# Performance work log

Measured on AMD Instinct MI355X. Metric: run time of the kernel, lower is better.

Reference implementation:

```python
import jax, jax.numpy as jnp
import numpy as np

B, L, H, HKV, D, E = 2, 2048, 8, 1, 256, 2048
SCALING = D ** -0.5


def rotate_half(x):
    x1, x2 = jnp.split(x, 2, axis=-1)
    return jnp.concatenate([-x2, x1], axis=-1)


def setup_inputs() -> dict:
    key = jax.random.key(0)
    ks = jax.random.split(key, 5)
    hidden_states = jax.random.normal(ks[0], (B, L, E), jnp.float32)
    attention_mask = jnp.zeros((B, 1, 1, L, L), jnp.float32)  # additive mask (all visible)
    # standard RoPE tables, shape [L, D]
    inv_freq = 1.0 / (10000.0 ** (jnp.arange(0, D, 2, dtype=jnp.float32) / D))
    freqs = jnp.arange(L, dtype=jnp.float32)[:, None] * inv_freq[None, :]
    emb = jnp.concatenate([freqs, freqs], axis=-1)
    cos, sin = jnp.cos(emb), jnp.sin(emb)
    s = 0.02
    Wq = jax.random.normal(ks[1], (H * D, E), jnp.float32) * s
    Wk = jax.random.normal(ks[2], (HKV * D, E), jnp.float32) * s
    Wv = jax.random.normal(ks[3], (HKV * D, E), jnp.float32) * s
    Wo = jax.random.normal(ks[4], (E, H * D), jnp.float32) * s
    return {"hidden_states": hidden_states, "attention_mask": attention_mask,
            "cos": cos, "sin": sin, "Wq": Wq, "Wk": Wk, "Wv": Wv, "Wo": Wo}


def reference(hidden_states, attention_mask, cos, sin, Wq, Wk, Wv, Wo):
    b, l, _ = hidden_states.shape
    q = jnp.einsum('ble,de->bld', hidden_states, Wq)
    k = jnp.einsum('ble,de->bld', hidden_states, Wk)
    v = jnp.einsum('ble,de->bld', hidden_states, Wv)
    # q: [B, L, 1, H, D] -> transpose(1,3) -> [B, H, 1, L, D]
    q = jnp.transpose(q.reshape(b, l, 1, H, D), (0, 3, 2, 1, 4))
    # k, v: [B, 1, L, Hkv, D] -> transpose(2,3) -> [B, 1, Hkv, L, D]
    k = jnp.transpose(k.reshape(b, 1, l, HKV, D), (0, 1, 3, 2, 4))
    v = jnp.transpose(v.reshape(b, 1, l, HKV, D), (0, 1, 3, 2, 4))
    # RoPE (cos/sin broadcast over leading dims)
    q = q * cos + rotate_half(q) * sin
    k = k * cos + rotate_half(k) * sin
    # scores: [B, H, Hkv, L, L]
    attn = jnp.matmul(q, jnp.swapaxes(k, -1, -2)) * SCALING
    attn = attn + attention_mask
    attn = jax.nn.softmax(attn.astype(jnp.float32), axis=-1)
    out = jnp.matmul(attn, v)                         # [B, H, Hkv, L, D]
    out = jnp.transpose(out, (0, 1, 3, 2, 4))         # [B, H, L, Hkv, D]
    out = out.reshape(b, l, H * D)                    # row-major reshape, as torch .reshape
    return jnp.einsum('bld,ed->ble', out, Wo)
```

## Files before the change

### kernel.cpp

```cpp
#include <hip/hip_runtime.h>

typedef unsigned short u16;
typedef __attribute__((ext_vector_type(8))) short short8;
typedef __attribute__((ext_vector_type(4))) float f32x4;
typedef __attribute__((ext_vector_type(16))) float f32x16;

struct __align__(8) US4 { u16 x, y, z, w; };

__device__ __forceinline__ u16 f2bf(float x) {
  union { float f; unsigned u; } c; c.f = x;
  unsigned r = c.u + 0x7fffu + ((c.u >> 16) & 1u);
  return (u16)(r >> 16);
}
__device__ __forceinline__ float bf2f(u16 u) {
  union { unsigned u; float f; } c; c.u = ((unsigned)u) << 16;
  return c.f;
}
__device__ __forceinline__ void gload_lds16(const void* g, void* l) {
  __builtin_amdgcn_global_load_lds(
      (const __attribute__((address_space(1))) void*)g,
      (__attribute__((address_space(3))) void*)l, 16, 0, 0);
}
__device__ __forceinline__ f32x4 fzero4() {
  f32x4 z; z[0] = 0.f; z[1] = 0.f; z[2] = 0.f; z[3] = 0.f; return z;
}
__device__ __forceinline__ unsigned cvtpk(float lo, float hi) {
  unsigned r;
  asm("v_cvt_pk_bf16_f32 %0, %1, %2" : "=v"(r) : "v"(lo), "v"(hi));
  return r;
}

__global__ __launch_bounds__(256) void cvt_all(
    const float* __restrict__ h, const float* __restrict__ wq,
    const float* __restrict__ wk, const float* __restrict__ wv,
    const float* __restrict__ wo, u16* __restrict__ Xbf,
    u16* __restrict__ Wqkv, u16* __restrict__ Wob) {
  int b = blockIdx.x;
  const float* s; u16* d; int off;
  if (b < 8192)       { s = h;  d = Xbf;            off = b; }
  else if (b < 12288) { s = wq; d = Wqkv;           off = b - 8192; }
  else if (b < 12800) { s = wk; d = Wqkv + 4194304; off = b - 12288; }
  else if (b < 13312) { s = wv; d = Wqkv + 4718592; off = b - 12800; }
  else                { s = wo; d = Wob;            off = b - 13312; }
  int i = (off * 256 + threadIdx.x) * 4;
  float4 v = *(const float4*)(s + i);
  US4 o = { f2bf(v.x), f2bf(v.y), f2bf(v.z), f2bf(v.w) };
  *(US4*)(d + i) = o;
}

template <int MODE>
__global__ __launch_bounds__(256) void gemm_nt(
    const u16* __restrict__ A, const u16* __restrict__ Bw,
    u16* __restrict__ q_out, u16* __restrict__ k_out, u16* __restrict__ v_out,
    float* __restrict__ c_out) {
  __shared__ u16 lA[128 * 32];
  __shared__ u16 lB[128 * 32];
  const int K = 2048;
  int t = threadIdx.x, w = t >> 6, lane = t & 63;
  int wm = w >> 1, wn = w & 1;

  int gx = gridDim.x;
  int wg = blockIdx.y * gx + blockIdx.x;
  int per = (gx * gridDim.y) >> 3;
  int nid = (wg & 7) * per + (wg >> 3);
  int m0 = (nid % gx) * 128, n0 = (nid / gx) * 128;

  int g = lane >> 4, qi = lane & 15;

  f32x4 acc[4][4];
#pragma unroll
  for (int i = 0; i < 4; i++)
#pragma unroll
    for (int j = 0; j < 4; j++) acc[i][j] = fzero4();

  for (int k0 = 0; k0 < K; k0 += 32) {
#pragma unroll
    for (int i = 0; i < 2; i++) {
      int off = i * 4096 + w * 1024 + lane * 16;
      int row = off >> 6, cg = (off >> 4) & 3;
      gload_lds16(A + (size_t)(m0 + row) * K + k0 + cg * 8,
                  (char*)lA + i * 4096 + w * 1024);
      gload_lds16(Bw + (size_t)(n0 + row) * K + k0 + cg * 8,
                  (char*)lB + i * 4096 + w * 1024);
    }
    __syncthreads();
    short8 af[4], bfr[4];
#pragma unroll
    for (int f = 0; f < 4; f++) {
      int ra = wm * 64 + f * 16 + qi;
      int rb = wn * 64 + f * 16 + qi;
      int kb2 = g * 16;
      af[f] = *(const short8*)((const char*)lA + ra * 64 + kb2);
      bfr[f] = *(const short8*)((const char*)lB + rb * 64 + kb2);
    }
#pragma unroll
    for (int i = 0; i < 4; i++)
#pragma unroll
      for (int j = 0; j < 4; j++)
        acc[i][j] = __builtin_amdgcn_mfma_f32_16x16x32_bf16(af[i], bfr[j], acc[i][j], 0, 0, 0);
    __syncthreads();
  }

#pragma unroll
  for (int i = 0; i < 4; i++) {
#pragma unroll
    for (int j = 0; j < 4; j++) {
#pragma unroll
      for (int r = 0; r < 4; r++) {
        int m = m0 + wm * 64 + i * 16 + g * 4 + r;
        int n = n0 + wn * 64 + j * 16 + qi;
        float v = acc[i][j][r];
        if (MODE == 0) {
          int b = m >> 11, l = m & 2047;
          if (n < 2048) {
            int hh = n >> 8, dd = n & 255;
            q_out[(((size_t)(b * 8 + hh) * 2048) + l) * 256 + dd] = f2bf(v);
          } else if (n < 2304) {
            int dd = n - 2048;
            k_out[((size_t)b * 2048 + l) * 256 + dd] = f2bf(v);
          } else {
            int dd = n - 2304;
            v_out[((size_t)b * 256 + dd) * 2048 + l] = f2bf(v);
          }
        } else {
          c_out[(size_t)m * 2048 + n] = v;
        }
      }
    }
  }
}

__global__ __launch_bounds__(256) void rope_kernel(u16* __restrict__ q, u16* __restrict__ k,
                                                   const float* __restrict__ cosT,
                                                   const float* __restrict__ sinT) {
  int idx = blockIdx.x * 2 + (threadIdx.x >> 7);
  int d = threadIdx.x & 127;
  u16* ptr;
  int l;
  float sc;
  if (idx < 32768) { ptr = q + (size_t)idx * 256; l = idx & 2047; sc = 0.0625f; }
  else             { ptr = k + (size_t)(idx - 32768) * 256; l = (idx - 32768) & 2047; sc = 1.0f; }
  float x1 = bf2f(ptr[d]), x2 = bf2f(ptr[d + 128]);
  float c1 = cosT[l * 256 + d], s1 = sinT[l * 256 + d];
  float c2 = cosT[l * 256 + d + 128], s2 = sinT[l * 256 + d + 128];
  float o1 = (x1 * c1 - x2 * s1) * sc;
  float o2 = (x2 * c2 + x1 * s2) * sc;
  ptr[d] = f2bf(o1);
  ptr[d + 128] = f2bf(o2);
}

__global__ __launch_bounds__(512, 2) void flash_kernel(
    const u16* __restrict__ qr, const u16* __restrict__ kr,
    const u16* __restrict__ vt_g, u16* __restrict__ attnout) {
  __shared__ __align__(16) char lds[147456];

  int t = threadIdx.x, w = t >> 6, lane = t & 63;
  int lo5 = lane & 31, hi = lane >> 5;
  int half = w >> 2, wl = w & 3;
  int b = blockIdx.z, h = blockIdx.y;
  int bh = b * 8 + h;
  int l0 = blockIdx.x * 128;
  int qrow = l0 + wl * 32 + lo5;

  const u16* kb = kr + (size_t)b * (2048 * 256);
  const u16* vb = vt_g + (size_t)b * (256 * 2048);
  char* unitbase = lds + half * 65536;
  int kvbase = half * 1024;

  short8 qf[16];
  {
    const u16* qb = qr + ((size_t)bh * 2048 + qrow) * 256 + hi * 8;
#pragma unroll
    for (int ks = 0; ks < 16; ks++) qf[ks] = *(const short8*)(qb + ks * 16);
  }

  f32x16 ot[8];
#pragma unroll
  for (int dv = 0; dv < 8; dv++)
#pragma unroll
    for (int r = 0; r < 16; r++) ot[dv][r] = 0.f;
  float mrow = -1e30f, lrow = 0.f;

  auto stage = [&](int buf, int it) {
    char* unit = unitbase + buf * 32768;
    int kvg = kvbase + it * 32;
#pragma unroll
    for (int i = 0; i < 4; i++) {
      int dbase = i * 4096 + wl * 1024;
      int off = dbase + lane * 16;
      {
        int row = off >> 9, slot = (off >> 4) & 31, ss = slot ^ (row & 7);
        gload_lds16(kb + (size_t)(kvg + row) * 256 + ss * 8, unit + dbase);
      }
      {
        int dd = off >> 6, slot = (off >> 4) & 3, ss = slot ^ ((dd >> 1) & 3);
        gload_lds16(vb + (size_t)dd * 2048 + kvg + ss * 8, unit + 16384 + dbase);
      }
    }
  };

  stage(0, 0);
  __syncthreads();

  for (int it = 0; it < 32; ++it) {
    int buf = it & 1;
    if (it < 31) stage(buf ^ 1, it + 1);
    char* unit = unitbase + buf * 32768;

    f32x16 st;
#pragma unroll
    for (int r = 0; r < 16; r++) st[r] = 0.f;
    __builtin_amdgcn_s_setprio(1);
#pragma unroll
    for (int ks = 0; ks < 16; ks++) {
      int ss = (2 * ks + hi) ^ (lo5 & 7);
      short8 kf = *(const short8*)(unit + lo5 * 512 + ss * 16);
      st = __builtin_amdgcn_mfma_f32_32x32x16_bf16(kf, qf[ks], st, 0, 0, 0);
    }
    __builtin_amdgcn_s_setprio(0);

    float tmax = st[0];
#pragma unroll
    for (int r = 1; r < 16; r++) tmax = fmaxf(tmax, st[r]);
    tmax = fmaxf(tmax, __shfl_xor(tmax, 32));
    if (__any(tmax > mrow)) {
      float mnew = fmaxf(mrow, tmax);
      float scale = __expf(mrow - mnew);
#pragma unroll
      for (int dv = 0; dv < 8; dv++)
#pragma unroll
        for (int r = 0; r < 16; r++) ot[dv][r] *= scale;
      lrow *= scale;
      mrow = mnew;
    }
    float tsum = 0.f;
#pragma unroll
    for (int r = 0; r < 16; r++) {
      float p = __expf(st[r] - mrow);
      st[r] = p;
      tsum += p;
    }
    tsum += __shfl_xor(tsum, 32);
    lrow += tsum;

#pragma unroll
    for (int jks = 0; jks < 2; jks++) {
      union { unsigned u[4]; short8 s; } pfu;
      {
        unsigned a0 = cvtpk(st[8 * jks + 0], st[8 * jks + 1]);
        unsigned a1 = cvtpk(st[8 * jks + 2], st[8 * jks + 3]);
        unsigned b0 = cvtpk(st[8 * jks + 4], st[8 * jks + 5]);
        unsigned b1 = cvtpk(st[8 * jks + 6], st[8 * jks + 7]);
        asm("v_permlane32_swap_b32 %0, %1" : "+v"(a0), "+v"(b0));
        asm("v_permlane32_swap_b32 %0, %1" : "+v"(a1), "+v"(b1));
        pfu.u[0] = a0; pfu.u[1] = a1; pfu.u[2] = b0; pfu.u[3] = b1;
      }
      short8 pf = pfu.s;
      __builtin_amdgcn_s_setprio(1);
#pragma unroll
      for (int dv = 0; dv < 8; dv++) {
        int dd = dv * 32 + lo5;
        int ss = (2 * jks + hi) ^ ((dd >> 1) & 3);
        short8 vf = *(const short8*)(unit + 16384 + dd * 64 + ss * 16);
        ot[dv] = __builtin_amdgcn_mfma_f32_32x32x16_bf16(vf, pf, ot[dv], 0, 0, 0);
      }
      __builtin_amdgcn_s_setprio(0);
    }
    __syncthreads();
  }

  char* chunk = lds + wl * 32768;
  float* mlx = (float*)(lds + 131072 + wl * 4096);
  if (half == 0) {
#pragma unroll
    for (int dv = 0; dv < 8; dv++)
#pragma unroll
      for (int r4 = 0; r4 < 4; r4++) {
        f32x4 v;
        v[0] = ot[dv][4 * r4 + 0]; v[1] = ot[dv][4 * r4 + 1];
        v[2] = ot[dv][4 * r4 + 2]; v[3] = ot[dv][4 * r4 + 3];
        *(f32x4*)(chunk + ((dv * 4 + r4) * 64 + lane) * 16) = v;
      }
    mlx[lane * 2 + 0] = mrow;
    mlx[lane * 2 + 1] = lrow;
  }
  __syncthreads();
  if (half == 1) {
    float mA = mlx[lane * 2 + 0], lA = mlx[lane * 2 + 1];
    float m = fmaxf(mA, mrow);
    float cA = __expf(mA - m), cB = __expf(mrow - m);
    float linv = 1.f / (lA * cA + lrow * cB);
    u16* ob = attnout + ((size_t)bh * 2048 + qrow) * 256;
#pragma unroll
    for (int dv = 0; dv < 8; dv++)
#pragma unroll
      for (int r4 = 0; r4 < 4; r4++) {
        f32x4 oA = *(const f32x4*)(chunk + ((dv * 4 + r4) * 64 + lane) * 16);
        US4 o;
        o.x = f2bf((oA[0] * cA + ot[dv][4 * r4 + 0] * cB) * linv);
        o.y = f2bf((oA[1] * cA + ot[dv][4 * r4 + 1] * cB) * linv);
        o.z = f2bf((oA[2] * cA + ot[dv][4 * r4 + 2] * cB) * linv);
        o.w = f2bf((oA[3] * cA + ot[dv][4 * r4 + 3] * cB) * linv);
        *(US4*)(ob + dv * 32 + 8 * r4 + 4 * hi) = o;
      }
  }
}

extern "C" void kernel_launch(void* const* d_in, const int* in_sizes, int n_in,
                              void* d_out, int out_size, void* d_ws, size_t ws_size,
                              hipStream_t stream) {
  const float* hidden = (const float*)d_in[0];
  const float* cosT = (const float*)d_in[2];
  const float* sinT = (const float*)d_in[3];
  const float* Wq = (const float*)d_in[4];
  const float* Wk = (const float*)d_in[5];
  const float* Wv = (const float*)d_in[6];
  const float* Wo = (const float*)d_in[7];

  char* ws = (char*)d_ws;
  u16* Xbf  = (u16*)(ws + 0);
  u16* Wqkv = (u16*)(ws + 16777216);
  u16* Wob  = (u16*)(ws + 27262976);
  u16* qbuf = (u16*)(ws + 35651584);
  u16* kbuf = (u16*)(ws + 52428800);
  u16* vT   = (u16*)(ws + 54525952);
  u16* attn = (u16*)(ws + 56623104);
  float* out = (float*)d_out;

  cvt_all<<<17408, 256, 0, stream>>>(hidden, Wq, Wk, Wv, Wo, Xbf, Wqkv, Wob);
  gemm_nt<0><<<dim3(32, 20), 256, 0, stream>>>(Xbf, Wqkv, qbuf, kbuf, vT, nullptr);
  rope_kernel<<<18432, 256, 0, stream>>>(qbuf, kbuf, cosT, sinT);
  flash_kernel<<<dim3(16, 8, 2), 512, 0, stream>>>(qbuf, kbuf, vT, attn);
  gemm_nt<1><<<dim3(32, 16), 256, 0, stream>>>(attn, Wob, nullptr, nullptr, nullptr, out);
}
```

Before: 273.5 us.

## Shrink flash blocks to 64 query rows and drop LDS double buffering

The flash attention kernel now uses 256-thread blocks covering 64 query rows, launched as twice as many blocks. Each block keeps a single K/V tile buffer in about 65 KB of LDS instead of two buffers in 144 KB. This lets more blocks fit on a CU and spreads work over the GPU. In exchange, global-to-LDS staging no longer overlaps with compute, and each iteration adds a barrier, so latency hiding has to come from other resident blocks rather than from software pipelining.

```diff
diff --git a/kernel.cpp b/kernel.cpp
--- a/kernel.cpp
+++ b/kernel.cpp
@@ -149,22 +149,22 @@
   ptr[d + 128] = f2bf(o2);
 }
 
-__global__ __launch_bounds__(512, 2) void flash_kernel(
+__global__ __launch_bounds__(256, 2) void flash_kernel(
     const u16* __restrict__ qr, const u16* __restrict__ kr,
     const u16* __restrict__ vt_g, u16* __restrict__ attnout) {
-  __shared__ __align__(16) char lds[147456];
+  __shared__ __align__(16) char lds[66560];
 
   int t = threadIdx.x, w = t >> 6, lane = t & 63;
   int lo5 = lane & 31, hi = lane >> 5;
-  int half = w >> 2, wl = w & 3;
+  int half = w & 1, qsl = w >> 1;
   int b = blockIdx.z, h = blockIdx.y;
   int bh = b * 8 + h;
-  int l0 = blockIdx.x * 128;
-  int qrow = l0 + wl * 32 + lo5;
+  int l0 = blockIdx.x * 64;
+  int qrow = l0 + qsl * 32 + lo5;
 
   const u16* kb = kr + (size_t)b * (2048 * 256);
   const u16* vb = vt_g + (size_t)b * (256 * 2048);
-  char* unitbase = lds + half * 65536;
+  char* unit = lds + half * 32768;
   int kvbase = half * 1024;
 
   short8 qf[16];
@@ -181,32 +181,27 @@
     for (int r = 0; r < 16; r++) ot[dv][r] = 0.f;
   float mrow = -1e30f, lrow = 0.f;
 
-  auto stage = [&](int buf, int it) {
-    char* unit = unitbase + buf * 32768;
+  auto stage = [&](int it) {
     int kvg = kvbase + it * 32;
 #pragma unroll
-    for (int i = 0; i < 4; i++) {
-      int dbase = i * 4096 + wl * 1024;
-      int off = dbase + lane * 16;
+    for (int i = 0; i < 8; i++) {
+      int dbase = i * 2048 + qsl * 1024;
+      int o = dbase + lane * 16;
       {
-        int row = off >> 9, slot = (off >> 4) & 31, ss = slot ^ (row & 7);
+        int row = o >> 9, slot = (o >> 4) & 31, ss = slot ^ (row & 7);
         gload_lds16(kb + (size_t)(kvg + row) * 256 + ss * 8, unit + dbase);
       }
       {
-        int dd = off >> 6, slot = (off >> 4) & 3, ss = slot ^ ((dd >> 1) & 3);
+        int dd = o >> 6, slot = (o >> 4) & 3, ss = slot ^ ((dd >> 1) & 3);
         gload_lds16(vb + (size_t)dd * 2048 + kvg + ss * 8, unit + 16384 + dbase);
       }
     }
   };
 
-  stage(0, 0);
+  stage(0);
   __syncthreads();
 
   for (int it = 0; it < 32; ++it) {
-    int buf = it & 1;
-    if (it < 31) stage(buf ^ 1, it + 1);
-    char* unit = unitbase + buf * 32768;
-
     f32x16 st;
 #pragma unroll
     for (int r = 0; r < 16; r++) st[r] = 0.f;
@@ -266,11 +261,14 @@
       }
       __builtin_amdgcn_s_setprio(0);
     }
+
     __syncthreads();
-  }
-
-  char* chunk = lds + wl * 32768;
-  float* mlx = (float*)(lds + 131072 + wl * 4096);
+    if (it < 31) stage(it + 1);
+    __syncthreads();
+  }
+
+  char* chunk = lds + qsl * 32768;
+  float* mlxq = (float*)(lds + 65536) + qsl * 128;
   if (half == 0) {
 #pragma unroll
     for (int dv = 0; dv < 8; dv++)
@@ -281,12 +279,12 @@
         v[2] = ot[dv][4 * r4 + 2]; v[3] = ot[dv][4 * r4 + 3];
         *(f32x4*)(chunk + ((dv * 4 + r4) * 64 + lane) * 16) = v;
       }
-    mlx[lane * 2 + 0] = mrow;
-    mlx[lane * 2 + 1] = lrow;
+    mlxq[lane * 2 + 0] = mrow;
+    mlxq[lane * 2 + 1] = lrow;
   }
   __syncthreads();
   if (half == 1) {
-    float mA = mlx[lane * 2 + 0], lA = mlx[lane * 2 + 1];
+    float mA = mlxq[lane * 2 + 0], lA = mlxq[lane * 2 + 1];
     float m = fmaxf(mA, mrow);
     float cA = __expf(mA - m), cB = __expf(mrow - m);
     float linv = 1.f / (lA * cA + lrow * cB);
@@ -330,6 +328,6 @@
   cvt_all<<<17408, 256, 0, stream>>>(hidden, Wq, Wk, Wv, Wo, Xbf, Wqkv, Wob);
   gemm_nt<0><<<dim3(32, 20), 256, 0, stream>>>(Xbf, Wqkv, qbuf, kbuf, vT, nullptr);
   rope_kernel<<<18432, 256, 0, stream>>>(qbuf, kbuf, cosT, sinT);
-  flash_kernel<<<dim3(16, 8, 2), 512, 0, stream>>>(qbuf, kbuf, vT, attn);
+  flash_kernel<<<dim3(32, 8, 2), 256, 0, stream>>>(qbuf, kbuf, vT, attn);
   gemm_nt<1><<<dim3(32, 16), 256, 0, stream>>>(attn, Wob, nullptr, nullptr, nullptr, out);
 }
```

Result: slower. 304.8 us (+11.4%).
